# Kernel tuning notes

Hardware: AMD Instinct MI355X
Metric: run time of the kernel (lower is better)

Reference implementation:

```python
import jax, jax.numpy as jnp
import numpy as np

V, MAXLEN, D, I, C, L, S = 32000, 4096, 1024, 4096, 1024, 4, 4096


def setup_inputs() -> dict:
    key = jax.random.key(0)
    ks = jax.random.split(key, 20)
    sd = 0.02
    inp = {
        "input_indices": jax.random.randint(ks[0], (S,), 0, V),
        "emb": jax.random.normal(ks[1], (V, D), jnp.float32) * sd,
        "pos": jax.random.normal(ks[2], (MAXLEN, D), jnp.float32) * sd,
        "Wq": jax.random.normal(ks[3], (L, D, I), jnp.float32) * sd,
        "bq": jnp.zeros((L, I), jnp.float32),
        "Wk": jax.random.normal(ks[4], (L, D, I), jnp.float32) * sd,
        "bk": jnp.zeros((L, I), jnp.float32),
        "Wv": jax.random.normal(ks[5], (L, D, I), jnp.float32) * sd,
        "bv": jnp.zeros((L, I), jnp.float32),
        "Wo": jax.random.normal(ks[6], (L, I, D), jnp.float32) * sd,
        "bo": jnp.zeros((L, D), jnp.float32),
        "W1": jax.random.normal(ks[7], (L, D, I), jnp.float32) * sd,
        "b1": jnp.zeros((L, I), jnp.float32),
        "W2": jax.random.normal(ks[8], (L, I, D), jnp.float32) * sd,
        "b2": jnp.zeros((L, D), jnp.float32),
        "Wout": jax.random.normal(ks[9], (D, C), jnp.float32) * sd,
        "bout": jnp.zeros((C,), jnp.float32),
    }
    return inp


def reference(input_indices, emb, pos, Wq, bq, Wk, bk, Wv, bv, Wo, bo, W1, b1, W2, b2, Wout, bout):
    s = input_indices.shape[0]
    x = emb[input_indices] + pos[:s]  # [S, D]
    causal_mask = jnp.triu(jnp.ones((s, s), bool), k=1)  # True above diagonal -> masked
    scale = 1.0 / np.sqrt(Wq.shape[-1]).astype(np.float32)

    def layer(x, p):
        wq, bq_, wk, bk_, wv, bv_, wo, bo_, w1, b1_, w2, b2_ = p
        q = x @ wq + bq_  # [S, I]
        k = x @ wk + bk_
        v = x @ wv + bv_
        scores = (q @ k.T) * scale  # [S, S]
        scores = jnp.where(causal_mask, -jnp.inf, scores)
        attn = jax.nn.softmax(scores, axis=-1)
        r = x + (attn @ v) @ wo + bo_  # residual + attention output projection
        f = jnp.maximum(r @ w1 + b1_, 0.0) @ w2 + b2_  # ReLU FFN
        return r + f, attn

    x, attention_maps = jax.lax.scan(
        layer, x, (Wq, bq, Wk, bk, Wv, bv, Wo, bo, W1, b1, W2, b2)
    )
    logits = x @ Wout + bout  # [S, C]
    log_probs = jax.nn.log_softmax(logits, axis=-1)
    return log_probs, attention_maps  # [S, C], [L, S, S]
```

## Files before the change

### kernel.cpp

```cpp
#include <hip/hip_runtime.h>
#include <stdint.h>
#include <math.h>

#define S_ 4096
#define D_ 1024
#define I_ 4096
#define C_ 1024
#define L_ 4

typedef unsigned short u16;
typedef short bf16x8 __attribute__((ext_vector_type(8)));
typedef float f32x4 __attribute__((ext_vector_type(4)));

__device__ __forceinline__ u16 f2bf(float f) {
  union { float f; uint32_t u; } c; c.f = f;
  return (u16)((c.u + 0x7FFFu + ((c.u >> 16) & 1u)) >> 16);
}

__device__ __forceinline__ void gll16(const void* g, void* l) {
  __builtin_amdgcn_global_load_lds(
      (__attribute__((address_space(1))) void*)(g),
      (__attribute__((address_space(3))) void*)(l), 16, 0, 0);
}

#define BAR() asm volatile("s_barrier" ::: "memory")
#define WAITV(n) asm volatile("s_waitcnt vmcnt(" #n ")" ::: "memory")

__device__ __forceinline__ int xcd_swz(int orig, int nwg) {
  int q8 = nwg >> 3, r8 = nwg & 7;
  int xcd = orig & 7, rem = orig >> 3;
  return (xcd < r8 ? xcd * (q8 + 1) : r8 * (q8 + 1) + (xcd - r8) * q8) + rem;
}

__device__ __forceinline__ void gemm256_body(
    u16* sA, u16* sB,
    const u16* __restrict__ A, const u16* __restrict__ Bt,
    const float* __restrict__ bias, const float* __restrict__ resid,
    float* __restrict__ outF, u16* __restrict__ outB,
    int N, int K, float scale, int relu,
    int row0, int col0, int t0, int t1)
{
  int tid = threadIdx.x, l = tid & 63;
  int w = tid >> 6;
  int wr = w >> 2, wc = w & 3;
  int lrow = l & 15, lq = l >> 4;
  int hb = wc >> 1;
  int rx = lrow & 7;

  const u16* ap[2]; const u16* bp[2]; int dst[2];
#pragma unroll
  for (int u = 0; u < 2; ++u) {
    int c = u * 512 + tid;
    int row = c >> 3;
    int oct = (c & 7) ^ (row & 7);
    ap[u] = A + (size_t)(row0 + row) * K + oct * 8;
    bp[u] = Bt + (size_t)(col0 + row) * K + oct * 8;
    dst[u] = c * 8;
  }

#define STAGE_A(par, hh, t)                                                     \
  { _Pragma("unroll") for (int u = 0; u < 2; ++u)                               \
      gll16(ap[u] + (size_t)(hh) * 128 * K + (t) * 64,                          \
            &sA[((par) * 2 + (hh)) * 8192 + dst[u]]); }
#define STAGE_B(par, hh, t)                                                     \
  { _Pragma("unroll") for (int u = 0; u < 2; ++u)                               \
      gll16(bp[u] + (size_t)(hh) * 128 * K + (t) * 64,                          \
            &sB[((par) * 2 + (hh)) * 8192 + dst[u]]); }
#define LD_A(DST, par, mh)                                                      \
  { _Pragma("unroll") for (int mi = 0; mi < 4; ++mi)                            \
    _Pragma("unroll") for (int kc = 0; kc < 2; ++kc)                            \
      DST[mi][kc] = *(const bf16x8*)&sA[((par) * 2 + wr) * 8192 +               \
          ((mh) * 64 + mi * 16 + lrow) * 64 + (((kc * 4 + lq) ^ rx) * 8)]; }
#define LD_B(DST, par, nh)                                                      \
  { _Pragma("unroll") for (int nj = 0; nj < 2; ++nj)                            \
    _Pragma("unroll") for (int kc = 0; kc < 2; ++kc)                            \
      DST[nj][kc] = *(const bf16x8*)&sB[((par) * 2 + hb) * 8192 +               \
          ((wc & 1) * 64 + (nh) * 32 + nj * 16 + lrow) * 64 +                   \
          (((kc * 4 + lq) ^ rx) * 8)]; }

  f32x4 acc[8][4];
#pragma unroll
  for (int i = 0; i < 8; ++i)
#pragma unroll
    for (int j = 0; j < 4; ++j) {
      acc[i][j][0] = 0.f; acc[i][j][1] = 0.f; acc[i][j][2] = 0.f; acc[i][j][3] = 0.f;
    }

#define MM(AF, MB, NB)                                                          \
  { __builtin_amdgcn_s_setprio(1);                                             \
    _Pragma("unroll") for (int kc = 0; kc < 2; ++kc)                            \
    _Pragma("unroll") for (int mi = 0; mi < 4; ++mi)                            \
    _Pragma("unroll") for (int nj = 0; nj < 2; ++nj)                            \
      acc[(MB) + mi][(NB) + nj] = __builtin_amdgcn_mfma_f32_16x16x32_bf16(      \
          AF[mi][kc], bfv[nj][kc], acc[(MB) + mi][(NB) + nj], 0, 0, 0);         \
    __builtin_amdgcn_s_setprio(0); }

  bf16x8 afA[4][2], afB[4][2], bfv[2][2];

  STAGE_A(0, 0, t0); STAGE_A(0, 1, t0); STAGE_B(0, 0, t0); STAGE_B(0, 1, t0);
  STAGE_A(1, 0, t0 + 1); STAGE_A(1, 1, t0 + 1); STAGE_B(1, 0, t0 + 1);
  WAITV(6);
  BAR();

  for (int t = t0; t < t1; ++t) {
    int p = (t - t0) & 1;
    LD_A(afA, p, 0);
    LD_B(bfv, p, 0);
    LD_A(afB, p, 1);
    if (t + 1 < t1) STAGE_B(p ^ 1, 1, t + 1);
    BAR();
    MM(afA, 0, 0);
    BAR();
    if (t + 2 < t1) STAGE_A(p, 0, t + 2);
    BAR();
    MM(afB, 4, 0);
    BAR();
    LD_B(bfv, p, 1);
    if (t + 2 < t1) STAGE_A(p, 1, t + 2);
    BAR();
    MM(afB, 4, 2);
    BAR();
    if (t + 2 < t1) STAGE_B(p, 0, t + 2);
    BAR();
    MM(afA, 0, 2);
    if (t + 2 < t1) { WAITV(6); } else { WAITV(0); }
    BAR();
  }
#undef STAGE_A
#undef STAGE_B
#undef LD_A
#undef LD_B
#undef MM

  float biasv[4] = {0.f, 0.f, 0.f, 0.f};
  if (bias) {
#pragma unroll
    for (int j = 0; j < 4; ++j) biasv[j] = bias[col0 + wc * 64 + j * 16 + lrow];
  }
#pragma unroll
  for (int i = 0; i < 8; ++i) {
#pragma unroll
    for (int r = 0; r < 4; ++r) {
      int row = row0 + wr * 128 + i * 16 + lq * 4 + r;
      size_t ro = (size_t)row * N;
#pragma unroll
      for (int j = 0; j < 4; ++j) {
        int col = col0 + wc * 64 + j * 16 + lrow;
        float v = acc[i][j][r] * scale + biasv[j];
        if (resid) v += resid[ro + col];
        if (relu) v = fmaxf(v, 0.f);
        if (outF) outF[ro + col] = v;
        if (outB) outB[ro + col] = f2bf(v);
      }
    }
  }
}

__global__ __launch_bounds__(512, 2) void gemm256k(
    const u16* __restrict__ A, const u16* __restrict__ Bt,
    const float* __restrict__ bias, const float* __restrict__ resid,
    float* __restrict__ outF, u16* __restrict__ outB,
    int M, int N, int K, float scale, int flags, int k0, int k1)
{
  extern __shared__ char smem[];
  int wg = xcd_swz(blockIdx.x, gridDim.x);
  int nbx = N / 256;
  int br = wg / nbx, bc = wg % nbx;
  if (flags & 4) { int lim = (br + 1) * 256; if (lim < k1) k1 = lim; }
  gemm256_body((u16*)smem, (u16*)smem + 32768, A, Bt, bias, resid, outF, outB,
               N, K, scale, flags & 1, br * 256, bc * 256, k0 / 64, k1 / 64);
}

__global__ __launch_bounds__(512, 2) void gemm256_tri2(
    const u16* __restrict__ A, const u16* __restrict__ Bt,
    float* __restrict__ outF0, float* __restrict__ outF1,
    int K, float scale)
{
  extern __shared__ char smem[];
  int wg = xcd_swz(blockIdx.x, gridDim.x);
  int half = gridDim.x >> 1;
  int chunk = (wg >= half) ? 1 : 0;
  int tile = wg - chunk * half;
  int br = (int)((sqrtf(8.0f * (float)tile + 1.0f) - 1.0f) * 0.5f);
  while ((br + 1) * (br + 2) / 2 <= tile) ++br;
  while (br * (br + 1) / 2 > tile) --br;
  int bc = tile - br * (br + 1) / 2;
  int k0 = chunk ? K / 2 : 0;
  int k1 = chunk ? K : K / 2;
  gemm256_body((u16*)smem, (u16*)smem + 32768, A, Bt, nullptr, nullptr,
               chunk ? outF1 : outF0, nullptr,
               S_, K, scale, 0, br * 256, bc * 256, k0 / 64, k1 / 64);
}

__global__ __launch_bounds__(512, 2) void gemm256_ks4(
    const u16* __restrict__ A, const u16* __restrict__ Bt,
    float* __restrict__ pOut, int M, int N, int K)
{
  extern __shared__ char smem[];
  int wg = xcd_swz(blockIdx.x, gridDim.x);
  int chunk = wg & 3;
  int tile = wg >> 2;
  int nbx = N / 256;
  int br = tile / nbx, bc = tile % nbx;
  float* o = pOut + (size_t)chunk * M * N;
  int kq = K / 4;
  gemm256_body((u16*)smem, (u16*)smem + 32768, A, Bt, nullptr, nullptr,
               o, nullptr, N, K, 1.0f, 0,
               br * 256, bc * 256, (chunk * kq) / 64, ((chunk + 1) * kq) / 64);
}

__global__ __launch_bounds__(256) void combine4(
    const float* __restrict__ p, const float* __restrict__ bias,
    const float* __restrict__ resid, float* __restrict__ outF,
    u16* __restrict__ outB, int MN, int N)
{
  int i = (blockIdx.x * 256 + threadIdx.x) * 4;
  f32x4 v = *(const f32x4*)&p[i];
  v += *(const f32x4*)&p[MN + i];
  v += *(const f32x4*)&p[2 * MN + i];
  v += *(const f32x4*)&p[3 * MN + i];
  int col = i & (N - 1);
  v += *(const f32x4*)&bias[col];
  v += *(const f32x4*)&resid[i];
  *(f32x4*)&outF[i] = v;
  ushort4 b;
  b.x = f2bf(v[0]); b.y = f2bf(v[1]); b.z = f2bf(v[2]); b.w = f2bf(v[3]);
  *(ushort4*)&outB[i] = b;
}

template <int BM_, int BN_>
__global__ __launch_bounds__(256) void gemm_bt(
    const u16* __restrict__ A, const u16* __restrict__ Bt,
    const float* __restrict__ bias, const float* __restrict__ resid,
    float* __restrict__ outF, u16* __restrict__ outB,
    int M, int N, int K, float scale, int flags)
{
  constexpr int FM = BM_ / 32;
  constexpr int FN = BN_ / 32;
  constexpr int ALOADS = BM_ * 8 / 256;
  constexpr int BLOADS = BN_ * 8 / 256;
  constexpr int WROWS = BM_ / 2;
  constexpr int WCOLS = BN_ / 2;

  int wg = xcd_swz(blockIdx.x, gridDim.x);
  int nbx = N / BN_;
  int br = wg / nbx, bc = wg % nbx;

  int tid = threadIdx.x;
  int l = tid & 63, w = tid >> 6;
  int wr = w >> 1, wc = w & 1;
  int lrow = l & 15, lq = l >> 4;
  int row0 = br * BM_, col0 = bc * BN_;

  __shared__ u16 lA[2][BM_ * 64];
  __shared__ u16 lB[2][BN_ * 64];

  const u16* aptr[ALOADS];
  const u16* bptr[BLOADS];
#pragma unroll
  for (int t = 0; t < ALOADS; ++t) {
    int c = t * 256 + tid;
    int row = c >> 3;
    int oct = (c & 7) ^ (row & 7);
    aptr[t] = A + (size_t)(row0 + row) * K + oct * 8;
  }
#pragma unroll
  for (int t = 0; t < BLOADS; ++t) {
    int c = t * 256 + tid;
    int row = c >> 3;
    int oct = (c & 7) ^ (row & 7);
    bptr[t] = Bt + (size_t)(col0 + row) * K + oct * 8;
  }

#define STAGE(b, koff)                                                          \
  {                                                                             \
    _Pragma("unroll") for (int t = 0; t < ALOADS; ++t)                          \
        gll16(aptr[t] + (koff), &lA[b][(t * 256 + tid) * 8]);                   \
    _Pragma("unroll") for (int t = 0; t < BLOADS; ++t)                          \
        gll16(bptr[t] + (koff), &lB[b][(t * 256 + tid) * 8]);                   \
  }

  f32x4 acc[FM][FN];
#pragma unroll
  for (int i = 0; i < FM; ++i)
#pragma unroll
    for (int j = 0; j < FN; ++j) {
      acc[i][j][0] = 0.f; acc[i][j][1] = 0.f; acc[i][j][2] = 0.f; acc[i][j][3] = 0.f;
    }

  int ktiles = K / 64;
  int rxA = lrow & 7;

  STAGE(0, 0);
  __syncthreads();
  int cur = 0;
  for (int kt = 0; kt < ktiles; ++kt) {
    if (kt + 1 < ktiles) STAGE(cur ^ 1, (kt + 1) * 64);
#pragma unroll
    for (int kc = 0; kc < 2; ++kc) {
      int kq = kc * 4 + lq;
      int octA = (kq ^ rxA) * 8;
      bf16x8 af[FM], bfv[FN];
#pragma unroll
      for (int i = 0; i < FM; ++i)
        af[i] = *(const bf16x8*)&lA[cur][(wr * WROWS + i * 16 + lrow) * 64 + octA];
#pragma unroll
      for (int j = 0; j < FN; ++j)
        bfv[j] = *(const bf16x8*)&lB[cur][(wc * WCOLS + j * 16 + lrow) * 64 + octA];
#pragma unroll
      for (int i = 0; i < FM; ++i)
#pragma unroll
        for (int j = 0; j < FN; ++j)
          acc[i][j] = __builtin_amdgcn_mfma_f32_16x16x32_bf16(af[i], bfv[j], acc[i][j], 0, 0, 0);
    }
    __syncthreads();
    cur ^= 1;
  }
#undef STAGE

  float biasv[FN];
#pragma unroll
  for (int j = 0; j < FN; ++j) biasv[j] = 0.f;
  if (bias) {
#pragma unroll
    for (int j = 0; j < FN; ++j) biasv[j] = bias[col0 + wc * WCOLS + j * 16 + lrow];
  }
  bool do_relu = (flags & 1) != 0;
#pragma unroll
  for (int i = 0; i < FM; ++i) {
#pragma unroll
    for (int r = 0; r < 4; ++r) {
      int row = row0 + wr * WROWS + i * 16 + lq * 4 + r;
      size_t ro = (size_t)row * N;
#pragma unroll
      for (int j = 0; j < FN; ++j) {
        int col = col0 + wc * WCOLS + j * 16 + lrow;
        float v = acc[i][j][r] * scale + biasv[j];
        if (resid) v += resid[ro + col];
        if (do_relu) v = fmaxf(v, 0.f);
        if (outF) outF[ro + col] = v;
        if (outB) outB[ro + col] = f2bf(v);
      }
    }
  }
}

struct T6 {
  const float* src[6];
  u16* dst[6];
};

__global__ __launch_bounds__(256) void trans6_f2b(T6 a) {
  __shared__ float tile[32][33];
  int z = blockIdx.z;
  bool big = (z == 3 || z == 5);
  int R = big ? I_ : D_;
  int C = big ? D_ : I_;
  int bid = blockIdx.y * gridDim.x + blockIdx.x;
  int nbx = C / 32;
  int bx = bid % nbx, by = bid / nbx;
  const float* src = a.src[z];
  u16* dst = a.dst[z];
  int c0 = bx * 32, r0 = by * 32;
  int tx = threadIdx.x & 31, ty = threadIdx.x >> 5;
#pragma unroll
  for (int i = 0; i < 32; i += 8)
    tile[ty + i][tx] = src[(size_t)(r0 + ty + i) * C + c0 + tx];
  __syncthreads();
#pragma unroll
  for (int i = 0; i < 32; i += 8)
    dst[(size_t)(c0 + ty + i) * R + r0 + tx] = f2bf(tile[tx][ty + i]);
}

__global__ __launch_bounds__(256) void trans_f2b(const float* __restrict__ src,
                                                 u16* __restrict__ dst, int R, int C)
{
  __shared__ float tile[32][33];
  int c0 = blockIdx.x * 32, r0 = blockIdx.y * 32;
  int tx = threadIdx.x & 31, ty = threadIdx.x >> 5;
#pragma unroll
  for (int i = 0; i < 32; i += 8)
    tile[ty + i][tx] = src[(size_t)(r0 + ty + i) * C + c0 + tx];
  __syncthreads();
#pragma unroll
  for (int i = 0; i < 32; i += 8)
    dst[(size_t)(c0 + ty + i) * R + r0 + tx] = f2bf(tile[tx][ty + i]);
}

__global__ __launch_bounds__(256) void trans_b2b(const u16* __restrict__ src,
                                                 u16* __restrict__ dst, int R, int C)
{
  __shared__ u16 tile[64][68];
  int c0 = blockIdx.x * 64, r0 = blockIdx.y * 64;
  int tx = threadIdx.x & 63, ty = threadIdx.x >> 6;
#pragma unroll
  for (int i = 0; i < 64; i += 4)
    tile[ty + i][tx] = src[(size_t)(r0 + ty + i) * C + c0 + tx];
  __syncthreads();
#pragma unroll
  for (int i = 0; i < 64; i += 4)
    dst[(size_t)(c0 + ty + i) * R + r0 + tx] = tile[tx][ty + i];
}

__global__ __launch_bounds__(256) void embed_k(const int* __restrict__ idx,
                                               const float* __restrict__ emb,
                                               const float* __restrict__ pos,
                                               float* __restrict__ xf, u16* __restrict__ xb)
{
  int s = blockIdx.y;
  int d = blockIdx.x * 256 + threadIdx.x;
  float v = emb[(size_t)idx[s] * D_ + d] + pos[(size_t)s * D_ + d];
  size_t o = (size_t)s * D_ + d;
  xf[o] = v;
  xb[o] = f2bf(v);
}

__global__ __launch_bounds__(256) void softmax_causal(float* __restrict__ att,
                                                      const float* __restrict__ attP1,
                                                      u16* __restrict__ attB)
{
  int s = blockIdx.x;
  __shared__ float row[S_];
  __shared__ float red[8];
  int tid = threadIdx.x, l = tid & 63, w = tid >> 6;
  int nv = s + 1;
  size_t base = (size_t)s * S_;
  float m = -3.0e38f;
  for (int c = tid; c < nv; c += 256) {
    float v = att[base + c] + attP1[base + c];
    row[c] = v; m = fmaxf(m, v);
  }
#pragma unroll
  for (int off = 32; off; off >>= 1) m = fmaxf(m, __shfl_xor(m, off, 64));
  if (l == 0) red[w] = m;
  __syncthreads();
  m = fmaxf(fmaxf(red[0], red[1]), fmaxf(red[2], red[3]));
  float sum = 0.f;
  for (int c = tid; c < nv; c += 256) { float e = __expf(row[c] - m); row[c] = e; sum += e; }
#pragma unroll
  for (int off = 32; off; off >>= 1) sum += __shfl_xor(sum, off, 64);
  if (l == 0) red[4 + w] = sum;
  __syncthreads();
  sum = red[4] + red[5] + red[6] + red[7];
  float inv = 1.0f / sum;
  int nb = ((s >> 8) + 1) * 256;
  for (int c = tid; c < S_; c += 256) {
    float p = (c < nv) ? row[c] * inv : 0.0f;
    att[base + c] = p;
    if (c < nb) attB[base + c] = f2bf(p);
  }
}

__global__ __launch_bounds__(256) void logsoftmax_k(const float* __restrict__ logits,
                                                    float* __restrict__ out)
{
  int s = blockIdx.x;
  int tid = threadIdx.x, l = tid & 63, w = tid >> 6;
  __shared__ float red[8];
  size_t base = (size_t)s * C_;
  float v[4];
  float m = -3.0e38f;
#pragma unroll
  for (int k = 0; k < 4; ++k) { v[k] = logits[base + tid + k * 256]; m = fmaxf(m, v[k]); }
#pragma unroll
  for (int off = 32; off; off >>= 1) m = fmaxf(m, __shfl_xor(m, off, 64));
  if (l == 0) red[w] = m;
  __syncthreads();
  m = fmaxf(fmaxf(red[0], red[1]), fmaxf(red[2], red[3]));
  float sum = 0.f;
#pragma unroll
  for (int k = 0; k < 4; ++k) sum += __expf(v[k] - m);
#pragma unroll
  for (int off = 32; off; off >>= 1) sum += __shfl_xor(sum, off, 64);
  if (l == 0) red[4 + w] = sum;
  __syncthreads();
  sum = red[4] + red[5] + red[6] + red[7];
  float lz = logf(sum);
#pragma unroll
  for (int k = 0; k < 4; ++k) out[base + tid + k * 256] = v[k] - m - lz;
}

extern "C" void kernel_launch(void* const* d_in, const int* in_sizes, int n_in,
                              void* d_out, int out_size, void* d_ws, size_t ws_size,
                              hipStream_t stream) {
  (void)in_sizes; (void)n_in; (void)out_size; (void)ws_size;
  const int*   idx  = (const int*)d_in[0];
  const float* emb  = (const float*)d_in[1];
  const float* pos  = (const float*)d_in[2];
  const float* Wq   = (const float*)d_in[3];
  const float* bq   = (const float*)d_in[4];
  const float* Wk   = (const float*)d_in[5];
  const float* bk   = (const float*)d_in[6];
  const float* Wv   = (const float*)d_in[7];
  const float* bv   = (const float*)d_in[8];
  const float* Wo   = (const float*)d_in[9];
  const float* bo   = (const float*)d_in[10];
  const float* W1   = (const float*)d_in[11];
  const float* b1   = (const float*)d_in[12];
  const float* W2   = (const float*)d_in[13];
  const float* b2   = (const float*)d_in[14];
  const float* Wout = (const float*)d_in[15];
  const float* bout = (const float*)d_in[16];
  float* out = (float*)d_out;

  char* ws = (char*)d_ws;
  const size_t MB = 1024ull * 1024ull;
  float* xres  = (float*)(ws + 0);
  u16*  xbf    = (u16*)(ws + 16 * MB);
  u16*  bufQ   = (u16*)(ws + 24 * MB);
  u16*  bufK   = (u16*)(ws + 56 * MB);
  u16*  bufV   = (u16*)(ws + 88 * MB);
  u16*  bufVT  = (u16*)(ws + 120 * MB);
  u16*  attnB  = (u16*)(ws + 152 * MB);
  float* logit = (float*)(ws + 184 * MB);
  u16* WqT   = (u16*)(ws + 200 * MB);
  u16* WkT   = (u16*)(ws + 208 * MB);
  u16* WvT   = (u16*)(ws + 216 * MB);
  u16* WoT   = (u16*)(ws + 224 * MB);
  u16* W1T   = (u16*)(ws + 232 * MB);
  u16* W2T   = (u16*)(ws + 240 * MB);
  u16* WoutT = (u16*)(ws + 248 * MB);
  float* attP1 = (float*)(ws + 256 * MB);
  float* pK    = (float*)(ws + 320 * MB);

  const float iscale = 1.0f / 64.0f;
  const int LDSB = 131072;
  hipFuncSetAttribute((const void*)gemm256k,
                      hipFuncAttributeMaxDynamicSharedMemorySize, LDSB);
  hipFuncSetAttribute((const void*)gemm256_tri2,
                      hipFuncAttributeMaxDynamicSharedMemorySize, LDSB);
  hipFuncSetAttribute((const void*)gemm256_ks4,
                      hipFuncAttributeMaxDynamicSharedMemorySize, LDSB);
  const int G_SQ = (S_ / 256) * (I_ / 256);
  const int G_TRI2 = (S_ / 256) * (S_ / 256 + 1);

  embed_k<<<dim3(D_ / 256, S_), 256, 0, stream>>>(idx, emb, pos, xres, xbf);

  for (int layer = 0; layer < L_; ++layer) {
    T6 t6;
    t6.src[0] = Wq + (size_t)layer * D_ * I_; t6.dst[0] = WqT;
    t6.src[1] = Wk + (size_t)layer * D_ * I_; t6.dst[1] = WkT;
    t6.src[2] = Wv + (size_t)layer * D_ * I_; t6.dst[2] = WvT;
    t6.src[3] = Wo + (size_t)layer * I_ * D_; t6.dst[3] = WoT;
    t6.src[4] = W1 + (size_t)layer * D_ * I_; t6.dst[4] = W1T;
    t6.src[5] = W2 + (size_t)layer * I_ * D_; t6.dst[5] = W2T;
    trans6_f2b<<<dim3(128, 32, 6), 256, 0, stream>>>(t6);

    gemm256k<<<G_SQ, 512, LDSB, stream>>>(
        xbf, WqT, bq + (size_t)layer * I_, nullptr, nullptr, bufQ,
        S_, I_, D_, 1.0f, 0, 0, D_);
    gemm256k<<<G_SQ, 512, LDSB, stream>>>(
        xbf, WkT, bk + (size_t)layer * I_, nullptr, nullptr, bufK,
        S_, I_, D_, 1.0f, 0, 0, D_);
    gemm256k<<<G_SQ, 512, LDSB, stream>>>(
        xbf, WvT, bv + (size_t)layer * I_, nullptr, nullptr, bufV,
        S_, I_, D_, 1.0f, 0, 0, D_);

    trans_b2b<<<dim3(I_ / 64, S_ / 64), 256, 0, stream>>>(bufV, bufVT, S_, I_);

    float* attL = out + (size_t)S_ * C_ + (size_t)layer * S_ * S_;
    gemm256_tri2<<<G_TRI2, 512, LDSB, stream>>>(bufQ, bufK, attL, attP1, I_, iscale);

    softmax_causal<<<S_, 256, 0, stream>>>(attL, attP1, attnB);

    gemm256k<<<G_SQ, 512, LDSB, stream>>>(
        attnB, bufVT, nullptr, nullptr, nullptr, bufQ,
        S_, I_, S_, 1.0f, 4, 0, S_);

    gemm256_ks4<<<(S_ / 256) * (D_ / 256) * 4, 512, LDSB, stream>>>(
        bufQ, WoT, pK, S_, D_, I_);
    combine4<<<(S_ * D_) / 1024, 256, 0, stream>>>(
        pK, bo + (size_t)layer * D_, xres, xres, xbf, S_ * D_, D_);

    gemm256k<<<G_SQ, 512, LDSB, stream>>>(
        xbf, W1T, b1 + (size_t)layer * I_, nullptr, nullptr, bufK,
        S_, I_, D_, 1.0f, 1, 0, D_);

    gemm256_ks4<<<(S_ / 256) * (D_ / 256) * 4, 512, LDSB, stream>>>(
        bufK, W2T, pK, S_, D_, I_);
    combine4<<<(S_ * D_) / 1024, 256, 0, stream>>>(
        pK, b2 + (size_t)layer * D_, xres, xres, xbf, S_ * D_, D_);
  }

  trans_f2b<<<dim3(C_ / 32, D_ / 32), 256, 0, stream>>>(Wout, WoutT, D_, C_);
  gemm_bt<64, 128><<<(S_ / 64) * (C_ / 128), 256, 0, stream>>>(
      xbf, WoutT, bout, nullptr, logit, nullptr, S_, C_, D_, 1.0f, 0);
  logsoftmax_k<<<S_, 256, 0, stream>>>(logit, out);
}
```

Baseline: 2.377 ms.

## Fuse QKV GEMMs, split QK^T three ways, split-K causal PV

Merges the three Q/K/V projection GEMMs into one 768-block launch, relying on WqT/WkT/WvT and bufQ/bufK/bufV being laid out contiguously in the workspace. Splits the causal QK^T along K into three chunks instead of two, and the softmax now sums three partials. Rebalances the causal P·V GEMM so that the heavier lower row blocks are split-K in two and then combined. The aim is fewer launches and better CU load balance on triangular work, at the cost of extra fp32 partial traffic and a combine kernel.

```diff
diff --git a/kernel.cpp b/kernel.cpp
--- a/kernel.cpp
+++ b/kernel.cpp
@@ -166,30 +166,82 @@
   int wg = xcd_swz(blockIdx.x, gridDim.x);
   int nbx = N / 256;
   int br = wg / nbx, bc = wg % nbx;
-  if (flags & 4) { int lim = (br + 1) * 256; if (lim < k1) k1 = lim; }
   gemm256_body((u16*)smem, (u16*)smem + 32768, A, Bt, bias, resid, outF, outB,
                N, K, scale, flags & 1, br * 256, bc * 256, k0 / 64, k1 / 64);
 }
 
-__global__ __launch_bounds__(512, 2) void gemm256_tri2(
-    const u16* __restrict__ A, const u16* __restrict__ Bt,
-    float* __restrict__ outF0, float* __restrict__ outF1,
-    int K, float scale)
+struct B3 { const float* b[3]; };
+__global__ __launch_bounds__(512, 2) void gemm256_qkv(
+    const u16* __restrict__ A, const u16* __restrict__ BtBase,
+    B3 b3, u16* __restrict__ outBase, int K)
 {
   extern __shared__ char smem[];
   int wg = xcd_swz(blockIdx.x, gridDim.x);
-  int half = gridDim.x >> 1;
-  int chunk = (wg >= half) ? 1 : 0;
-  int tile = wg - chunk * half;
+  int z = wg >> 8;
+  int tile = wg & 255;
+  int br = tile >> 4, bc = tile & 15;
+  gemm256_body((u16*)smem, (u16*)smem + 32768, A,
+               BtBase + (size_t)z * I_ * D_, b3.b[z], nullptr,
+               nullptr, outBase + (size_t)z * S_ * I_,
+               I_, K, 1.0f, 0, br * 256, bc * 256, 0, K / 64);
+}
+
+__global__ __launch_bounds__(512, 2) void gemm256_tri3(
+    const u16* __restrict__ A, const u16* __restrict__ Bt,
+    float* __restrict__ out0, float* __restrict__ out1, float* __restrict__ out2,
+    int K, float scale)
+{
+  extern __shared__ char smem[];
+  int wg = xcd_swz(blockIdx.x, gridDim.x);
+  int ntri = gridDim.x / 3;
+  int chunk = wg / ntri;
+  int tile = wg - chunk * ntri;
   int br = (int)((sqrtf(8.0f * (float)tile + 1.0f) - 1.0f) * 0.5f);
   while ((br + 1) * (br + 2) / 2 <= tile) ++br;
   while (br * (br + 1) / 2 > tile) --br;
   int bc = tile - br * (br + 1) / 2;
-  int k0 = chunk ? K / 2 : 0;
-  int k1 = chunk ? K : K / 2;
+  int t0 = (chunk == 0) ? 0 : (chunk == 1 ? 22 : 43);
+  int t1 = (chunk == 0) ? 22 : (chunk == 1 ? 43 : 64);
+  float* o = (chunk == 0) ? out0 : (chunk == 1 ? out1 : out2);
   gemm256_body((u16*)smem, (u16*)smem + 32768, A, Bt, nullptr, nullptr,
-               chunk ? outF1 : outF0, nullptr,
-               S_, K, scale, 0, br * 256, bc * 256, k0 / 64, k1 / 64);
+               o, nullptr, S_, K, scale, 0, br * 256, bc * 256, t0, t1);
+}
+
+__global__ __launch_bounds__(512, 2) void gemm256_pv(
+    const u16* __restrict__ A, const u16* __restrict__ Bt,
+    u16* __restrict__ outB, float* __restrict__ pv)
+{
+  extern __shared__ char smem[];
+  int wg = xcd_swz(blockIdx.x, gridDim.x);
+  if (wg < 128) {
+    int br = wg >> 4, bc = wg & 15;
+    gemm256_body((u16*)smem, (u16*)smem + 32768, A, Bt, nullptr, nullptr,
+                 nullptr, outB, I_, S_, 1.0f, 0,
+                 br * 256, bc * 256, 0, (br + 1) * 4);
+  } else {
+    int c = wg - 128;
+    int br = 8 + (c >> 5);
+    int bc = (c >> 1) & 15;
+    int chunk = c & 1;
+    int lim = (br + 1) * 4;
+    int half = lim >> 1;
+    float* o = pv + (size_t)chunk * (S_ / 2) * I_ - (size_t)2048 * I_;
+    gemm256_body((u16*)smem, (u16*)smem + 32768, A, Bt, nullptr, nullptr,
+                 o, nullptr, I_, S_, 1.0f, 0,
+                 br * 256, bc * 256, chunk ? half : 0, chunk ? lim : half);
+  }
+}
+
+__global__ __launch_bounds__(256) void combine2pv(
+    const float* __restrict__ pv, u16* __restrict__ outB)
+{
+  const int MN = (S_ / 2) * I_;
+  int i = (blockIdx.x * 256 + threadIdx.x) * 4;
+  f32x4 v = *(const f32x4*)&pv[i];
+  v += *(const f32x4*)&pv[MN + i];
+  ushort4 b;
+  b.x = f2bf(v[0]); b.y = f2bf(v[1]); b.z = f2bf(v[2]); b.w = f2bf(v[3]);
+  *(ushort4*)&outB[(size_t)2048 * I_ + i] = b;
 }
 
 __global__ __launch_bounds__(512, 2) void gemm256_ks4(
@@ -417,6 +469,7 @@
 
 __global__ __launch_bounds__(256) void softmax_causal(float* __restrict__ att,
                                                       const float* __restrict__ attP1,
+                                                      const float* __restrict__ attP2,
                                                       u16* __restrict__ attB)
 {
   int s = blockIdx.x;
@@ -427,7 +480,7 @@
   size_t base = (size_t)s * S_;
   float m = -3.0e38f;
   for (int c = tid; c < nv; c += 256) {
-    float v = att[base + c] + attP1[base + c];
+    float v = att[base + c] + attP1[base + c] + attP2[base + c];
     row[c] = v; m = fmaxf(m, v);
   }
 #pragma unroll
@@ -527,12 +580,15 @@
   const int LDSB = 131072;
   hipFuncSetAttribute((const void*)gemm256k,
                       hipFuncAttributeMaxDynamicSharedMemorySize, LDSB);
-  hipFuncSetAttribute((const void*)gemm256_tri2,
+  hipFuncSetAttribute((const void*)gemm256_qkv,
+                      hipFuncAttributeMaxDynamicSharedMemorySize, LDSB);
+  hipFuncSetAttribute((const void*)gemm256_tri3,
+                      hipFuncAttributeMaxDynamicSharedMemorySize, LDSB);
+  hipFuncSetAttribute((const void*)gemm256_pv,
                       hipFuncAttributeMaxDynamicSharedMemorySize, LDSB);
   hipFuncSetAttribute((const void*)gemm256_ks4,
                       hipFuncAttributeMaxDynamicSharedMemorySize, LDSB);
   const int G_SQ = (S_ / 256) * (I_ / 256);
-  const int G_TRI2 = (S_ / 256) * (S_ / 256 + 1);
 
   embed_k<<<dim3(D_ / 256, S_), 256, 0, stream>>>(idx, emb, pos, xres, xbf);
 
@@ -546,26 +602,22 @@
     t6.src[5] = W2 + (size_t)layer * I_ * D_; t6.dst[5] = W2T;
     trans6_f2b<<<dim3(128, 32, 6), 256, 0, stream>>>(t6);
 
-    gemm256k<<<G_SQ, 512, LDSB, stream>>>(
-        xbf, WqT, bq + (size_t)layer * I_, nullptr, nullptr, bufQ,
-        S_, I_, D_, 1.0f, 0, 0, D_);
-    gemm256k<<<G_SQ, 512, LDSB, stream>>>(
-        xbf, WkT, bk + (size_t)layer * I_, nullptr, nullptr, bufK,
-        S_, I_, D_, 1.0f, 0, 0, D_);
-    gemm256k<<<G_SQ, 512, LDSB, stream>>>(
-        xbf, WvT, bv + (size_t)layer * I_, nullptr, nullptr, bufV,
-        S_, I_, D_, 1.0f, 0, 0, D_);
+    B3 b3;
+    b3.b[0] = bq + (size_t)layer * I_;
+    b3.b[1] = bk + (size_t)layer * I_;
+    b3.b[2] = bv + (size_t)layer * I_;
+    gemm256_qkv<<<3 * G_SQ, 512, LDSB, stream>>>(xbf, WqT, b3, bufQ, D_);
 
     trans_b2b<<<dim3(I_ / 64, S_ / 64), 256, 0, stream>>>(bufV, bufVT, S_, I_);
 
     float* attL = out + (size_t)S_ * C_ + (size_t)layer * S_ * S_;
-    gemm256_tri2<<<G_TRI2, 512, LDSB, stream>>>(bufQ, bufK, attL, attP1, I_, iscale);
-
-    softmax_causal<<<S_, 256, 0, stream>>>(attL, attP1, attnB);
-
-    gemm256k<<<G_SQ, 512, LDSB, stream>>>(
-        attnB, bufVT, nullptr, nullptr, nullptr, bufQ,
-        S_, I_, S_, 1.0f, 4, 0, S_);
+    gemm256_tri3<<<3 * 136, 512, LDSB, stream>>>(bufQ, bufK, attL, attP1, pK,
+                                                 I_, iscale);
+
+    softmax_causal<<<S_, 256, 0, stream>>>(attL, attP1, pK, attnB);
+
+    gemm256_pv<<<384, 512, LDSB, stream>>>(attnB, bufVT, bufQ, attP1);
+    combine2pv<<<(S_ / 2) * (I_ / 1024), 256, 0, stream>>>(attP1, bufQ);
 
     gemm256_ks4<<<(S_ / 256) * (D_ / 256) * 4, 512, LDSB, stream>>>(
         bufQ, WoT, pK, S_, D_, I_);
```

Measured after the change: 2.283 ms. 4.0% less time.
